# Kernel optimization log

Hardware: AMD Instinct MI355X
Metric: run time of the kernel (lower is better)

Reference implementation:

```python
import jax, jax.numpy as jnp
import numpy as np

T, B, E, H = 2048, 2, 1024, 16
DH = E // H  # head_dim = 64


def setup_inputs() -> dict:
    key = jax.random.key(0)
    ks = jax.random.split(key, 5)
    query = jax.random.normal(ks[0], (T, B, E), dtype=jnp.float32)
    # self-attention: key/value are passed but unused by the module
    k_in = query
    v_in = query
    # xavier-ish scaled params
    in_proj_weight = jax.random.normal(ks[1], (3 * E, E), dtype=jnp.float32) * (E ** -0.5)
    in_proj_bias = jnp.zeros((3 * E,), dtype=jnp.float32)
    out_w = jax.random.normal(ks[2], (E, E), dtype=jnp.float32) * (E ** -0.5)
    out_b = jnp.zeros((E,), dtype=jnp.float32)
    return {"query": query, "key": k_in, "value": v_in,
            "in_proj_weight": in_proj_weight, "in_proj_bias": in_proj_bias,
            "out_w": out_w, "out_b": out_b}


def reference(query, key, value, in_proj_weight, in_proj_bias, out_w, out_b):
    # query: [T, B, E] (fairseq Time x Batch x Channel)
    t, b, e = query.shape
    scaling = DH ** -0.5
    # fused QKV projection: in_proj_weight [3E, E]
    qkv = jnp.einsum('tbe,fe->tbf', query, in_proj_weight) + in_proj_bias  # [T,B,3E]
    q, k, v = jnp.split(qkv, 3, axis=-1)
    q = q * scaling
    # split heads -> [T, B, H, DH]
    q = q.reshape(t, b, H, DH)
    k = k.reshape(t, b, H, DH)
    v = v.reshape(t, b, H, DH)
    # attention scores [B, H, T, T]
    scores = jnp.einsum('tbhd,sbhd->bhts', q, k)
    probs = jax.nn.softmax(scores, axis=-1)
    # weighted sum -> [T, B, H, DH] -> [T, B, E]
    attn = jnp.einsum('bhts,sbhd->tbhd', probs, v).reshape(t, b, e)
    # output projection (LinearSuper with sample dims == super dims)
    out = jnp.einsum('tbe,oe->tbo', attn, out_w) + out_b
    return out
```

## Files before the change

### kernel.cpp

```cpp
#include <hip/hip_runtime.h>
#include <hip/hip_bf16.h>
#include <stdint.h>
#include <math.h>

#define T_DIM 2048
#define B_DIM 2
#define E_DIM 1024
#define H_DIM 16
#define DH    64
#define MROWS (T_DIM * B_DIM)
#define QKVN  (3 * E_DIM)

typedef __attribute__((ext_vector_type(8))) __bf16 bf16x8;
typedef __attribute__((ext_vector_type(4))) float f32x4;
typedef __attribute__((ext_vector_type(4))) uint32_t u32x4;
typedef __attribute__((ext_vector_type(2))) uint32_t u32x2;

typedef __attribute__((address_space(1))) const uint32_t gu32;
typedef __attribute__((address_space(3))) uint32_t lu32;

#define GLL(gp, lp) __builtin_amdgcn_global_load_lds((gu32*)(gp), (lu32*)(lp), 16, 0, 0)

#define QSCALE 0.18033688011112042f

#if __has_builtin(__builtin_amdgcn_exp2f)
#define EXP2(x) __builtin_amdgcn_exp2f(x)
#else
#define EXP2(x) exp2f(x)
#endif

static __device__ __forceinline__ unsigned short f2bf(float f) {
    uint32_t u = __float_as_uint(f);
    u += 0x7FFFu + ((u >> 16) & 1u);
    return (unsigned short)(u >> 16);
}

__global__ void k_cvt3(const float* __restrict__ q,  const float* __restrict__ w,
                       const float* __restrict__ o,
                       unsigned short* __restrict__ qo, unsigned short* __restrict__ wo,
                       unsigned short* __restrict__ oo) {
    long i = (long)(blockIdx.x * 256 + threadIdx.x) * 8;
    const float* src; unsigned short* dst; long off;
    if (i < 4194304)      { src = q; dst = qo; off = i; }
    else if (i < 7340032) { src = w; dst = wo; off = i - 4194304; }
    else                  { src = o; dst = oo; off = i - 7340032; }
    float4 a = *(const float4*)(src + off);
    float4 b = *(const float4*)(src + off + 4);
    union { unsigned short s[8]; u32x4 v; } r;
    r.s[0] = f2bf(a.x); r.s[1] = f2bf(a.y); r.s[2] = f2bf(a.z); r.s[3] = f2bf(a.w);
    r.s[4] = f2bf(b.x); r.s[5] = f2bf(b.y); r.s[6] = f2bf(b.z); r.s[7] = f2bf(b.w);
    *(u32x4*)(dst + off) = r.v;
}

template <int STORE_BF16, int SCALE_Q>
__global__ __launch_bounds__(256) void k_gemm_bt(
    const unsigned short* __restrict__ A,
    const unsigned short* __restrict__ B,
    const float* __restrict__ bias,
    void* __restrict__ C,
    int M, int N, int K)
{
    __shared__ unsigned short As[128 * 64];
    __shared__ unsigned short Bs[128 * 64];
    const int tid = threadIdx.x;
    const int wid = tid >> 6, lane = tid & 63;
    const int m0 = blockIdx.y * 128, n0 = blockIdx.x * 128;

    const unsigned short* ag[4];
    const unsigned short* bg[4];
    unsigned lo[4];
#pragma unroll
    for (int j = 0; j < 4; ++j) {
        int o = (wid * 4 + j) * 1024 + lane * 16;
        int r = o >> 7;
        int c = (o >> 4) & 7;
        int cs = (c ^ (r & 7)) * 8;
        ag[j] = A + (long)(m0 + r) * K + cs;
        bg[j] = B + (long)(n0 + r) * K + cs;
        lo[j] = (unsigned)((wid * 4 + j) * 1024);
    }

    f32x4 acc[4][4] = {};
    const int wr = wid >> 1, wc = wid & 1;
    const int nk = K >> 6;

    for (int kt = 0; kt < nk; ++kt) {
#pragma unroll
        for (int j = 0; j < 4; ++j) {
            GLL(ag[j], (char*)As + lo[j]);
            GLL(bg[j], (char*)Bs + lo[j]);
            ag[j] += 64;
            bg[j] += 64;
        }
        __syncthreads();

        bf16x8 af[4][2], bfr[4][2];
#pragma unroll
        for (int i = 0; i < 4; ++i) {
            int ra = wr * 64 + i * 16 + (lane & 15);
            int rb = wc * 64 + i * 16 + (lane & 15);
#pragma unroll
            for (int kk = 0; kk < 2; ++kk) {
                int sa = ((kk * 4 + (lane >> 4)) ^ (ra & 7)) * 16;
                int sb = ((kk * 4 + (lane >> 4)) ^ (rb & 7)) * 16;
                af[i][kk]  = *(const bf16x8*)((char*)As + ra * 128 + sa);
                bfr[i][kk] = *(const bf16x8*)((char*)Bs + rb * 128 + sb);
            }
        }
#pragma unroll
        for (int kk = 0; kk < 2; ++kk)
#pragma unroll
            for (int mi = 0; mi < 4; ++mi)
#pragma unroll
                for (int ni = 0; ni < 4; ++ni)
                    acc[mi][ni] = __builtin_amdgcn_mfma_f32_16x16x32_bf16(
                        af[mi][kk], bfr[ni][kk], acc[mi][ni], 0, 0, 0);
        __syncthreads();
    }

#pragma unroll
    for (int mi = 0; mi < 4; ++mi)
#pragma unroll
        for (int ni = 0; ni < 4; ++ni) {
            int col = n0 + wc * 64 + ni * 16 + (lane & 15);
            float bv = bias[col];
            float scl = (SCALE_Q && col < 1024) ? QSCALE : 1.0f;
#pragma unroll
            for (int r = 0; r < 4; ++r) {
                int row = m0 + wr * 64 + mi * 16 + (lane >> 4) * 4 + r;
                float v = (acc[mi][ni][r] + bv) * scl;
                if (STORE_BF16)
                    ((unsigned short*)C)[(long)row * N + col] = f2bf(v);
                else
                    ((float*)C)[(long)row * N + col] = v;
            }
        }
}

__global__ __launch_bounds__(256) void k_transpose_v(
    const unsigned short* __restrict__ qkv, unsigned short* __restrict__ Vt)
{
    __shared__ unsigned short tile[64 * 64];
    const int bh = blockIdx.x >> 5, tt = blockIdx.x & 31;
    const int b = bh >> 4, h = bh & 15;
    const int tid = threadIdx.x;

    {
        int tr = tid >> 3;
        int s0 = tid & 7;
#pragma unroll
        for (int rr = 0; rr < 2; ++rr) {
            int t = tr + rr * 32;
            u32x4 v = *(const u32x4*)(qkv + ((long)(tt * 64 + t) * 2 + b) * 3072 + 2048 + h * 64 + s0 * 8);
            int slot = s0 ^ (t & 7) ^ ((t >> 3) & 7);
            *(u32x4*)((char*)tile + t * 128 + slot * 16) = v;
        }
    }
    __syncthreads();
    {
        int d = tid >> 3;
        int t8 = (tid & 7) * 8;
#pragma unroll
        for (int rr = 0; rr < 2; ++rr) {
            int dd = d + rr * 32;
            union { unsigned short s[8]; u32x4 v; } r;
#pragma unroll
            for (int i = 0; i < 8; ++i) {
                int pos = t8 + i;
                int t = 4 * ((pos >> 3) & 3) + (pos & 3) + 16 * (2 * (pos >> 5) + ((pos >> 2) & 1));
                int slot = (dd >> 3) ^ (t & 7) ^ ((t >> 3) & 7);
                r.s[i] = *(const unsigned short*)((char*)tile + t * 128 + slot * 16 + (dd & 7) * 2);
            }
            *(u32x4*)(Vt + ((long)bh * 64 + dd) * 2048 + tt * 64 + t8) = r.v;
        }
    }
}

__global__ __launch_bounds__(256, 2) void k_attn(
    const unsigned short* __restrict__ qkv,
    const unsigned short* __restrict__ Vt,
    unsigned short* __restrict__ attn)
{
    __shared__ unsigned short Ks[2 * 64 * 64];
    __shared__ unsigned short Vs[2 * 64 * 64];
    const int tid = threadIdx.x, wid = tid >> 6, lane = tid & 63;
    const int bh = blockIdx.x >> 4, tq = blockIdx.x & 15;
    const int b = bh >> 4, h = bh & 15;

    bf16x8 qf[2][2];
#pragma unroll
    for (int mi = 0; mi < 2; ++mi)
#pragma unroll
        for (int kk = 0; kk < 2; ++kk) {
            int t = tq * 128 + wid * 32 + mi * 16 + (lane & 15);
            qf[mi][kk] = *(const bf16x8*)(qkv + (long)(t * 2 + b) * 3072 + h * 64 + kk * 32 + (lane >> 4) * 8);
        }

    const unsigned short* kg[2];
    const unsigned short* vg[2];
    unsigned lo[2];
#pragma unroll
    for (int j = 0; j < 2; ++j) {
        int o = (wid * 2 + j) * 1024 + lane * 16;
        int r = o >> 7, c = (o >> 4) & 7;
        int cs = (c ^ (r & 7)) * 8;
        kg[j] = qkv + (long)(r * 2 + b) * 3072 + 1024 + h * 64 + cs;
        vg[j] = Vt + ((long)bh * 64 + r) * 2048 + cs;
        lo[j] = (unsigned)((wid * 2 + j) * 1024);
    }

    f32x4 acc[2][4] = {};
    float suma[2] = {0.f, 0.f};

#pragma unroll
    for (int j = 0; j < 2; ++j) {
        GLL(kg[j], (char*)Ks + lo[j]);
        GLL(vg[j], (char*)Vs + lo[j]);
        kg[j] += 64 * 6144;
        vg[j] += 64;
    }

    for (int st = 0; st < 32; ++st) {
        const int cur = st & 1;
        if (st < 31) {
#pragma unroll
            for (int j = 0; j < 2; ++j) {
                GLL(kg[j], (char*)Ks + (cur ^ 1) * 8192 + lo[j]);
                GLL(vg[j], (char*)Vs + (cur ^ 1) * 8192 + lo[j]);
                kg[j] += 64 * 6144;
                vg[j] += 64;
            }
            asm volatile("s_waitcnt vmcnt(4)" ::: "memory");
        } else {
            asm volatile("s_waitcnt vmcnt(0)" ::: "memory");
        }
        __builtin_amdgcn_s_barrier();

        const char* kbase = (const char*)Ks + cur * 8192;
        const char* vbase = (const char*)Vs + cur * 8192;

        bf16x8 kf[4][2];
#pragma unroll
        for (int ni = 0; ni < 4; ++ni) {
            int row = ni * 16 + (lane & 15);
#pragma unroll
            for (int kk = 0; kk < 2; ++kk) {
                int sl = ((kk * 4 + (lane >> 4)) ^ (row & 7)) * 16;
                kf[ni][kk] = *(const bf16x8*)(kbase + row * 128 + sl);
            }
        }
        f32x4 sc[2][4] = {};
#pragma unroll
        for (int kk = 0; kk < 2; ++kk)
#pragma unroll
            for (int mi = 0; mi < 2; ++mi)
#pragma unroll
                for (int ni = 0; ni < 4; ++ni)
                    sc[mi][ni] = __builtin_amdgcn_mfma_f32_16x16x32_bf16(
                        kf[ni][kk], qf[mi][kk], sc[mi][ni], 0, 0, 0);

        bf16x8 pfrag[2][2];
#pragma unroll
        for (int mi = 0; mi < 2; ++mi) {
            float ex[4][4];
            float part = 0.f;
#pragma unroll
            for (int ni = 0; ni < 4; ++ni)
#pragma unroll
                for (int r = 0; r < 4; ++r) {
                    float e = EXP2(sc[mi][ni][r]);
                    ex[ni][r] = e;
                    part += e;
                }
            suma[mi] += part;
#pragma unroll
            for (int a = 0; a < 2; ++a) {
                union { uint32_t u[4]; bf16x8 v; } pk;
                pk.u[0] = (uint32_t)f2bf(ex[2 * a][0])     | ((uint32_t)f2bf(ex[2 * a][1]) << 16);
                pk.u[1] = (uint32_t)f2bf(ex[2 * a][2])     | ((uint32_t)f2bf(ex[2 * a][3]) << 16);
                pk.u[2] = (uint32_t)f2bf(ex[2 * a + 1][0]) | ((uint32_t)f2bf(ex[2 * a + 1][1]) << 16);
                pk.u[3] = (uint32_t)f2bf(ex[2 * a + 1][2]) | ((uint32_t)f2bf(ex[2 * a + 1][3]) << 16);
                pfrag[mi][a] = pk.v;
            }
        }

        bf16x8 vf[4][2];
#pragma unroll
        for (int nd = 0; nd < 4; ++nd) {
            int row = nd * 16 + (lane & 15);
#pragma unroll
            for (int a = 0; a < 2; ++a) {
                int sl = ((a * 4 + (lane >> 4)) ^ (row & 7)) * 16;
                vf[nd][a] = *(const bf16x8*)(vbase + row * 128 + sl);
            }
        }
#pragma unroll
        for (int a = 0; a < 2; ++a)
#pragma unroll
            for (int mi = 0; mi < 2; ++mi)
#pragma unroll
                for (int nd = 0; nd < 4; ++nd)
                    acc[mi][nd] = __builtin_amdgcn_mfma_f32_16x16x32_bf16(
                        vf[nd][a], pfrag[mi][a], acc[mi][nd], 0, 0, 0);
        __builtin_amdgcn_s_barrier();
    }

#pragma unroll
    for (int mi = 0; mi < 2; ++mi) {
        suma[mi] += __shfl_xor(suma[mi], 16, 64);
        suma[mi] += __shfl_xor(suma[mi], 32, 64);
    }

#pragma unroll
    for (int mi = 0; mi < 2; ++mi) {
        float inv = 1.0f / suma[mi];
        int t = tq * 128 + wid * 32 + mi * 16 + (lane & 15);
#pragma unroll
        for (int nd = 0; nd < 4; ++nd) {
            int e = h * 64 + nd * 16 + (lane >> 4) * 4;
            u32x2 w;
            w.x = (uint32_t)f2bf(acc[mi][nd][0] * inv) | ((uint32_t)f2bf(acc[mi][nd][1] * inv) << 16);
            w.y = (uint32_t)f2bf(acc[mi][nd][2] * inv) | ((uint32_t)f2bf(acc[mi][nd][3] * inv) << 16);
            *(u32x2*)(attn + (long)(t * 2 + b) * 1024 + e) = w;
        }
    }
}

extern "C" void kernel_launch(void* const* d_in, const int* in_sizes, int n_in,
                              void* d_out, int out_size, void* d_ws, size_t ws_size,
                              hipStream_t stream) {
    const float* query = (const float*)d_in[0];
    const float* ipw   = (const float*)d_in[3];
    const float* ipb   = (const float*)d_in[4];
    const float* ow    = (const float*)d_in[5];
    const float* ob    = (const float*)d_in[6];
    float* out = (float*)d_out;

    char* ws = (char*)d_ws;
    unsigned short* Xb   = (unsigned short*)(ws);
    unsigned short* Wb   = (unsigned short*)(ws + (8l << 20));
    unsigned short* OWb  = (unsigned short*)(ws + (14l << 20));
    unsigned short* qkvp = (unsigned short*)(ws + (16l << 20));
    unsigned short* Vtp  = (unsigned short*)(ws + (40l << 20));
    unsigned short* attn = (unsigned short*)(ws + (48l << 20));

    k_cvt3<<<4096, 256, 0, stream>>>(query, ipw, ow, Xb, Wb, OWb);

    k_gemm_bt<1, 1><<<dim3(QKVN / 128, MROWS / 128), 256, 0, stream>>>(
        Xb, Wb, ipb, qkvp, MROWS, QKVN, E_DIM);

    k_transpose_v<<<1024, 256, 0, stream>>>(qkvp, Vtp);

    k_attn<<<512, 256, 0, stream>>>(qkvp, Vtp, attn);

    k_gemm_bt<0, 0><<<dim3(E_DIM / 128, MROWS / 128), 256, 0, stream>>>(
        attn, OWb, ob, out, MROWS, E_DIM, E_DIM);
}
```

Baseline: 223.2 us.

## Halve attention query tile per block and add MFMA priority hints

```diff
diff --git a/kernel.cpp b/kernel.cpp
--- a/kernel.cpp
+++ b/kernel.cpp
@@ -184,17 +184,15 @@
     __shared__ unsigned short Ks[2 * 64 * 64];
     __shared__ unsigned short Vs[2 * 64 * 64];
     const int tid = threadIdx.x, wid = tid >> 6, lane = tid & 63;
-    const int bh = blockIdx.x >> 4, tq = blockIdx.x & 15;
+    const int bh = blockIdx.x >> 5, tq = blockIdx.x & 31;
     const int b = bh >> 4, h = bh & 15;
 
-    bf16x8 qf[2][2];
-#pragma unroll
-    for (int mi = 0; mi < 2; ++mi)
-#pragma unroll
-        for (int kk = 0; kk < 2; ++kk) {
-            int t = tq * 128 + wid * 32 + mi * 16 + (lane & 15);
-            qf[mi][kk] = *(const bf16x8*)(qkv + (long)(t * 2 + b) * 3072 + h * 64 + kk * 32 + (lane >> 4) * 8);
-        }
+    bf16x8 qf[2];
+#pragma unroll
+    for (int kk = 0; kk < 2; ++kk) {
+        int t = tq * 64 + wid * 16 + (lane & 15);
+        qf[kk] = *(const bf16x8*)(qkv + (long)(t * 2 + b) * 3072 + h * 64 + kk * 32 + (lane >> 4) * 8);
+    }
 
     const unsigned short* kg[2];
     const unsigned short* vg[2];
@@ -209,8 +207,8 @@
         lo[j] = (unsigned)((wid * 2 + j) * 1024);
     }
 
-    f32x4 acc[2][4] = {};
-    float suma[2] = {0.f, 0.f};
+    f32x4 acc[4] = {};
+    float suma = 0.f;
 
 #pragma unroll
     for (int j = 0; j < 2; ++j) {
@@ -249,39 +247,36 @@
                 kf[ni][kk] = *(const bf16x8*)(kbase + row * 128 + sl);
             }
         }
-        f32x4 sc[2][4] = {};
+        f32x4 sc[4] = {};
+        __builtin_amdgcn_s_setprio(1);
 #pragma unroll
         for (int kk = 0; kk < 2; ++kk)
 #pragma unroll
-            for (int mi = 0; mi < 2; ++mi)
-#pragma unroll
-                for (int ni = 0; ni < 4; ++ni)
-                    sc[mi][ni] = __builtin_amdgcn_mfma_f32_16x16x32_bf16(
-                        kf[ni][kk], qf[mi][kk], sc[mi][ni], 0, 0, 0);
-
-        bf16x8 pfrag[2][2];
-#pragma unroll
-        for (int mi = 0; mi < 2; ++mi) {
-            float ex[4][4];
-            float part = 0.f;
-#pragma unroll
             for (int ni = 0; ni < 4; ++ni)
-#pragma unroll
-                for (int r = 0; r < 4; ++r) {
-                    float e = EXP2(sc[mi][ni][r]);
-                    ex[ni][r] = e;
-                    part += e;
-                }
-            suma[mi] += part;
-#pragma unroll
-            for (int a = 0; a < 2; ++a) {
-                union { uint32_t u[4]; bf16x8 v; } pk;
-                pk.u[0] = (uint32_t)f2bf(ex[2 * a][0])     | ((uint32_t)f2bf(ex[2 * a][1]) << 16);
-                pk.u[1] = (uint32_t)f2bf(ex[2 * a][2])     | ((uint32_t)f2bf(ex[2 * a][3]) << 16);
-                pk.u[2] = (uint32_t)f2bf(ex[2 * a + 1][0]) | ((uint32_t)f2bf(ex[2 * a + 1][1]) << 16);
-                pk.u[3] = (uint32_t)f2bf(ex[2 * a + 1][2]) | ((uint32_t)f2bf(ex[2 * a + 1][3]) << 16);
-                pfrag[mi][a] = pk.v;
-            }
+                sc[ni] = __builtin_amdgcn_mfma_f32_16x16x32_bf16(
+                    kf[ni][kk], qf[kk], sc[ni], 0, 0, 0);
+        __builtin_amdgcn_s_setprio(0);
+
+        float ex[4][4];
+        float part = 0.f;
+#pragma unroll
+        for (int ni = 0; ni < 4; ++ni)
+#pragma unroll
+            for (int r = 0; r < 4; ++r) {
+                float e = EXP2(sc[ni][r]);
+                ex[ni][r] = e;
+                part += e;
+            }
+        suma += part;
+        bf16x8 pfrag[2];
+#pragma unroll
+        for (int a = 0; a < 2; ++a) {
+            union { uint32_t u[4]; bf16x8 v; } pk;
+            pk.u[0] = (uint32_t)f2bf(ex[2 * a][0])     | ((uint32_t)f2bf(ex[2 * a][1]) << 16);
+            pk.u[1] = (uint32_t)f2bf(ex[2 * a][2])     | ((uint32_t)f2bf(ex[2 * a][3]) << 16);
+            pk.u[2] = (uint32_t)f2bf(ex[2 * a + 1][0]) | ((uint32_t)f2bf(ex[2 * a + 1][1]) << 16);
+            pk.u[3] = (uint32_t)f2bf(ex[2 * a + 1][2]) | ((uint32_t)f2bf(ex[2 * a + 1][3]) << 16);
+            pfrag[a] = pk.v;
         }
 
         bf16x8 vf[4][2];
@@ -294,33 +289,29 @@
                 vf[nd][a] = *(const bf16x8*)(vbase + row * 128 + sl);
             }
         }
+        __builtin_amdgcn_s_setprio(1);
 #pragma unroll
         for (int a = 0; a < 2; ++a)
 #pragma unroll
-            for (int mi = 0; mi < 2; ++mi)
-#pragma unroll
-                for (int nd = 0; nd < 4; ++nd)
-                    acc[mi][nd] = __builtin_amdgcn_mfma_f32_16x16x32_bf16(
-                        vf[nd][a], pfrag[mi][a], acc[mi][nd], 0, 0, 0);
+            for (int nd = 0; nd < 4; ++nd)
+                acc[nd] = __builtin_amdgcn_mfma_f32_16x16x32_bf16(
+                    vf[nd][a], pfrag[a], acc[nd], 0, 0, 0);
+        __builtin_amdgcn_s_setprio(0);
         __builtin_amdgcn_s_barrier();
     }
 
-#pragma unroll
-    for (int mi = 0; mi < 2; ++mi) {
-        suma[mi] += __shfl_xor(suma[mi], 16, 64);
-        suma[mi] += __shfl_xor(suma[mi], 32, 64);
-    }
-
-#pragma unroll
-    for (int mi = 0; mi < 2; ++mi) {
-        float inv = 1.0f / suma[mi];
-        int t = tq * 128 + wid * 32 + mi * 16 + (lane & 15);
+    suma += __shfl_xor(suma, 16, 64);
+    suma += __shfl_xor(suma, 32, 64);
+
+    {
+        float inv = 1.0f / suma;
+        int t = tq * 64 + wid * 16 + (lane & 15);
 #pragma unroll
         for (int nd = 0; nd < 4; ++nd) {
             int e = h * 64 + nd * 16 + (lane >> 4) * 4;
             u32x2 w;
-            w.x = (uint32_t)f2bf(acc[mi][nd][0] * inv) | ((uint32_t)f2bf(acc[mi][nd][1] * inv) << 16);
-            w.y = (uint32_t)f2bf(acc[mi][nd][2] * inv) | ((uint32_t)f2bf(acc[mi][nd][3] * inv) << 16);
+            w.x = (uint32_t)f2bf(acc[nd][0] * inv) | ((uint32_t)f2bf(acc[nd][1] * inv) << 16);
+            w.y = (uint32_t)f2bf(acc[nd][2] * inv) | ((uint32_t)f2bf(acc[nd][3] * inv) << 16);
             *(u32x2*)(attn + (long)(t * 2 + b) * 1024 + e) = w;
         }
     }
@@ -351,7 +342,7 @@
 
     k_transpose_v<<<1024, 256, 0, stream>>>(qkvp, Vtp);
 
-    k_attn<<<512, 256, 0, stream>>>(qkvp, Vtp, attn);
+    k_attn<<<1024, 256, 0, stream>>>(qkvp, Vtp, attn);
 
     k_gemm_bt<0, 0><<<dim3(E_DIM / 128, MROWS / 128), 256, 0, stream>>>(
         attn, OWb, ob, out, MROWS, E_DIM, E_DIM);
```

New measurement: 224.0 us. Within noise of the previous version (+0.4%).
